# Optimization experiments

Measured on AMD Instinct MI355X. Metric: run time of the kernel, lower is better.

Reference implementation:

```python
import jax, jax.numpy as jnp
import numpy as np

QMAX = 127.0  # int8 symmetric range


def _fake_quant(x, axes):
    """AQT-style int8 symmetric fake-quant over contraction axes.

    Returns quantized integer values (stored as f32) and per-channel scales
    (keepdims over `axes`).
    """
    absmax = jnp.max(jnp.abs(x), axis=axes, keepdims=True)
    scale = jnp.where(absmax > 0, absmax / QMAX, jnp.ones_like(absmax))
    q = jnp.clip(jnp.round(x / scale), -QMAX, QMAX)
    return q, scale


def setup_inputs() -> dict:
    key = jax.random.key(0)
    k1, k2 = jax.random.split(key)
    lhs = jax.random.normal(k1, (4, 16384, 512), dtype=jnp.float32)
    rhs = jax.random.normal(k2, (512, 512), dtype=jnp.float32)
    return {"lhs": lhs, "rhs": rhs}


def reference(lhs, rhs):
    # dimension_numbers = (((2,), (0,)), ((), ())) -- Dense-style contraction.
    # Quantize each operand symmetrically to int8 along its contraction axis.
    lhs_q, lhs_scale = _fake_quant(lhs, axes=(2,))   # lhs_q: [B,S,D], scale: [B,S,1]
    rhs_q, rhs_scale = _fake_quant(rhs, axes=(0,))   # rhs_q: [D,F], scale: [1,F]
    # Integer-valued matmul (accumulation exact in f32 for these magnitudes),
    # then dequantize with the outer product of scales.
    acc = jnp.einsum('bsd,df->bsf', lhs_q, rhs_q)    # [B,S,F]
    return acc * lhs_scale * rhs_scale               # broadcast [B,S,1]*[1,F]
```

## Files before the change

kernel.cpp:

```cpp
#include <hip/hip_runtime.h>
#include <hip/hip_bf16.h>
#include <stdint.h>

#define QMAX 127.0f

typedef __attribute__((ext_vector_type(4))) int i32x4;
typedef __attribute__((ext_vector_type(2))) int i32x2;

typedef __attribute__((address_space(1))) const void GVoid;
typedef __attribute__((address_space(3))) void LVoid;

__device__ inline int quant_i(float x, float inv) {
    float q = rintf(x * inv);
    q = fminf(fmaxf(q, -QMAX), QMAX);
    return (int)q;
}

__device__ inline uint32_t pack4(float4 v, float inv) {
    return (uint32_t)(quant_i(v.x, inv) & 255)
         | ((uint32_t)(quant_i(v.y, inv) & 255) << 8)
         | ((uint32_t)(quant_i(v.z, inv) & 255) << 16)
         | ((uint32_t)(quant_i(v.w, inv) & 255) << 24);
}

__device__ inline float amax8(float4 a, float4 b) {
    return fmaxf(fmaxf(fmaxf(fabsf(a.x), fabsf(a.y)), fmaxf(fabsf(a.z), fabsf(a.w))),
                 fmaxf(fmaxf(fabsf(b.x), fabsf(b.y)), fmaxf(fabsf(b.z), fabsf(b.w))));
}

__global__ void quant_rhs_kernel(const float* __restrict__ rhs,
                                 int8_t* __restrict__ Bt,
                                 float* __restrict__ rscale) {
    const int f = blockIdx.x;
    const int t = threadIdx.x;
    float v[8];
    float amax = 0.f;
#pragma unroll
    for (int i = 0; i < 8; ++i) {
        v[i] = rhs[(size_t)(t + 64 * i) * 512 + f];
        amax = fmaxf(amax, fabsf(v[i]));
    }
#pragma unroll
    for (int m = 1; m <= 32; m <<= 1)
        amax = fmaxf(amax, __shfl_xor(amax, m, 64));
    const float inv = amax > 0.f ? QMAX / amax : 0.f;
    if (t == 0) rscale[f] = amax > 0.f ? amax * (1.0f / QMAX) : 1.0f;
#pragma unroll
    for (int i = 0; i < 8; ++i)
        Bt[(size_t)f * 512 + t + 64 * i] = (int8_t)quant_i(v[i], inv);
}

__global__ __launch_bounds__(256, 8) void quant_lhs_kernel(const float* __restrict__ lhs,
                                                           int8_t* __restrict__ Aq,
                                                           float* __restrict__ lscale) {
    const int lane = threadIdx.x & 63;
    const int wave = threadIdx.x >> 6;
    const int row0 = blockIdx.x * 32 + wave * 8;
    const float* rp = lhs + (size_t)row0 * 512 + lane * 8;
    int8_t* op = Aq + (size_t)row0 * 512 + lane * 8;
#pragma unroll
    for (int r = 0; r < 8; r += 2) {
        const float4 a0 = *(const float4*)(rp + (size_t)r * 512);
        const float4 b0 = *(const float4*)(rp + (size_t)r * 512 + 4);
        const float4 a1 = *(const float4*)(rp + (size_t)(r + 1) * 512);
        const float4 b1 = *(const float4*)(rp + (size_t)(r + 1) * 512 + 4);
        float m0 = amax8(a0, b0);
        float m1 = amax8(a1, b1);
#pragma unroll
        for (int m = 1; m <= 32; m <<= 1) {
            m0 = fmaxf(m0, __shfl_xor(m0, m, 64));
            m1 = fmaxf(m1, __shfl_xor(m1, m, 64));
        }
        const float inv0 = m0 > 0.f ? QMAX / m0 : 0.f;
        const float inv1 = m1 > 0.f ? QMAX / m1 : 0.f;
        if (lane == 0) {
            lscale[row0 + r]     = m0 > 0.f ? m0 * (1.0f / QMAX) : 1.0f;
            lscale[row0 + r + 1] = m1 > 0.f ? m1 * (1.0f / QMAX) : 1.0f;
        }
        i32x2 p0, p1;
        p0.x = (int)pack4(a0, inv0); p0.y = (int)pack4(b0, inv0);
        p1.x = (int)pack4(a1, inv1); p1.y = (int)pack4(b1, inv1);
        *(i32x2*)(op + (size_t)r * 512)       = p0;
        *(i32x2*)(op + (size_t)(r + 1) * 512) = p1;
    }
}

__global__ __launch_bounds__(256, 3) void gemm_kernel(const int8_t* __restrict__ Aq,
                                                      const int8_t* __restrict__ Bt,
                                                      const float* __restrict__ lscale,
                                                      const float* __restrict__ rscale,
                                                      float* __restrict__ out) {
    __shared__ int8_t lds[32768];

    const int tid  = threadIdx.x;
    const int lane = tid & 63;
    const int wave = tid >> 6;
    const int wr   = wave >> 1;
    const int wc   = wave & 1;

    const int g   = blockIdx.x;
    const int xcd = g & 7;
    const int j   = g >> 3;
    const int m0  = (xcd * 64 + (j >> 2)) * 128;
    const int n0  = (j & 3) * 128;

    i32x4 acc[4][4];
#pragma unroll
    for (int i = 0; i < 4; ++i)
#pragma unroll
        for (int jj = 0; jj < 4; ++jj)
            acc[i][jj] = (i32x4){0, 0, 0, 0};

    const int lane15 = lane & 15;
    const int laneHi = lane >> 4;

#pragma unroll
    for (int kt = 0; kt < 512; kt += 128) {
        __syncthreads();
#pragma unroll
        for (int c = 0; c < 4; ++c) {
            const int chunk = (c * 4 + wave) * 1024;
            const int d     = chunk + lane * 16;
            const int row   = d >> 7;
            const int koff  = d & 127;
            const int srck  = koff ^ ((row & 7) << 4);
            const int8_t* srcA = Aq + (size_t)(m0 + row) * 512 + kt + srck;
            __builtin_amdgcn_global_load_lds((GVoid*)srcA, (LVoid*)(lds + chunk), 16, 0, 0);
            const int8_t* srcB = Bt + (size_t)(n0 + row) * 512 + kt + srck;
            __builtin_amdgcn_global_load_lds((GVoid*)srcB, (LVoid*)(lds + 16384 + chunk), 16, 0, 0);
        }
        __syncthreads();

        i32x4 af[4][2], bf[4][2];
#pragma unroll
        for (int mi = 0; mi < 4; ++mi) {
            const int row = wr * 64 + mi * 16 + lane15;
            const int sw  = (row & 7) << 4;
#pragma unroll
            for (int kk = 0; kk < 2; ++kk) {
                const int kb = kk * 64 + laneHi * 16;
                af[mi][kk] = *(const i32x4*)(lds + row * 128 + (kb ^ sw));
            }
        }
#pragma unroll
        for (int ni = 0; ni < 4; ++ni) {
            const int col = wc * 64 + ni * 16 + lane15;
            const int sw  = (col & 7) << 4;
#pragma unroll
            for (int kk = 0; kk < 2; ++kk) {
                const int kb = kk * 64 + laneHi * 16;
                bf[ni][kk] = *(const i32x4*)(lds + 16384 + col * 128 + (kb ^ sw));
            }
        }
#pragma unroll
        for (int kk = 0; kk < 2; ++kk)
#pragma unroll
            for (int mi = 0; mi < 4; ++mi)
#pragma unroll
                for (int ni = 0; ni < 4; ++ni)
                    acc[mi][ni] = __builtin_amdgcn_mfma_i32_16x16x64_i8(
                        af[mi][kk], bf[ni][kk], acc[mi][ni], 0, 0, 0);
    }

    float rs[4];
#pragma unroll
    for (int ni = 0; ni < 4; ++ni)
        rs[ni] = rscale[n0 + wc * 64 + ni * 16 + lane15];
    const int rg = laneHi * 4;
#pragma unroll
    for (int mi = 0; mi < 4; ++mi) {
#pragma unroll
        for (int r = 0; r < 4; ++r) {
            const int grow = m0 + wr * 64 + mi * 16 + rg + r;
            const float ls = lscale[grow];
            float* op = out + (size_t)grow * 512 + n0 + wc * 64;
#pragma unroll
            for (int ni = 0; ni < 4; ++ni)
                op[ni * 16 + lane15] = (float)acc[mi][ni][r] * ls * rs[ni];
        }
    }
}

extern "C" void kernel_launch(void* const* d_in, const int* in_sizes, int n_in,
                              void* d_out, int out_size, void* d_ws, size_t ws_size,
                              hipStream_t stream) {
    const float* lhs = (const float*)d_in[0];
    const float* rhs = (const float*)d_in[1];
    float* out = (float*)d_out;

    char* ws = (char*)d_ws;
    int8_t* Bt    = (int8_t*)ws;
    float* rscale = (float*)(ws + 262144);
    float* lscale = (float*)(ws + 266240);
    int8_t* Aq    = (int8_t*)(ws + 1048576);

    const int rows = in_sizes[0] / 512;

    quant_rhs_kernel<<<512, 64, 0, stream>>>(rhs, Bt, rscale);
    quant_lhs_kernel<<<rows / 32, 256, 0, stream>>>(lhs, Aq, lscale);
    gemm_kernel<<<(rows / 128) * 4, 256, 0, stream>>>(Aq, Bt, lscale, rscale, out);
}
```

Baseline: 73.21 us.

## Fuse quant kernels, double-buffer GEMM LDS, add nontemporal loads/stores

```diff
diff --git a/kernel.cpp b/kernel.cpp
--- a/kernel.cpp
+++ b/kernel.cpp
@@ -4,8 +4,9 @@
 
 #define QMAX 127.0f
 
-typedef __attribute__((ext_vector_type(4))) int i32x4;
-typedef __attribute__((ext_vector_type(2))) int i32x2;
+typedef __attribute__((ext_vector_type(4))) int   i32x4;
+typedef __attribute__((ext_vector_type(2))) int   i32x2;
+typedef __attribute__((ext_vector_type(4))) float f32x4v;
 
 typedef __attribute__((address_space(1))) const void GVoid;
 typedef __attribute__((address_space(3))) void LVoid;
@@ -16,54 +17,58 @@
     return (int)q;
 }
 
-__device__ inline uint32_t pack4(float4 v, float inv) {
+__device__ inline uint32_t pack4(f32x4v v, float inv) {
     return (uint32_t)(quant_i(v.x, inv) & 255)
          | ((uint32_t)(quant_i(v.y, inv) & 255) << 8)
          | ((uint32_t)(quant_i(v.z, inv) & 255) << 16)
          | ((uint32_t)(quant_i(v.w, inv) & 255) << 24);
 }
 
-__device__ inline float amax8(float4 a, float4 b) {
+__device__ inline float amax8(f32x4v a, f32x4v b) {
     return fmaxf(fmaxf(fmaxf(fabsf(a.x), fabsf(a.y)), fmaxf(fabsf(a.z), fabsf(a.w))),
                  fmaxf(fmaxf(fabsf(b.x), fabsf(b.y)), fmaxf(fabsf(b.z), fabsf(b.w))));
 }
 
-__global__ void quant_rhs_kernel(const float* __restrict__ rhs,
-                                 int8_t* __restrict__ Bt,
-                                 float* __restrict__ rscale) {
-    const int f = blockIdx.x;
-    const int t = threadIdx.x;
-    float v[8];
-    float amax = 0.f;
-#pragma unroll
-    for (int i = 0; i < 8; ++i) {
-        v[i] = rhs[(size_t)(t + 64 * i) * 512 + f];
-        amax = fmaxf(amax, fabsf(v[i]));
-    }
-#pragma unroll
-    for (int m = 1; m <= 32; m <<= 1)
-        amax = fmaxf(amax, __shfl_xor(amax, m, 64));
-    const float inv = amax > 0.f ? QMAX / amax : 0.f;
-    if (t == 0) rscale[f] = amax > 0.f ? amax * (1.0f / QMAX) : 1.0f;
-#pragma unroll
-    for (int i = 0; i < 8; ++i)
-        Bt[(size_t)f * 512 + t + 64 * i] = (int8_t)quant_i(v[i], inv);
-}
-
-__global__ __launch_bounds__(256, 8) void quant_lhs_kernel(const float* __restrict__ lhs,
-                                                           int8_t* __restrict__ Aq,
-                                                           float* __restrict__ lscale) {
+__global__ __launch_bounds__(256, 8) void quant_kernel(const float* __restrict__ lhs,
+                                                       const float* __restrict__ rhs,
+                                                       int8_t* __restrict__ Aq,
+                                                       int8_t* __restrict__ Bt,
+                                                       float* __restrict__ lscale,
+                                                       float* __restrict__ rscale,
+                                                       int nLhs) {
     const int lane = threadIdx.x & 63;
     const int wave = threadIdx.x >> 6;
-    const int row0 = blockIdx.x * 32 + wave * 8;
+    const int bid  = blockIdx.x;
+
+    if (bid >= nLhs) {
+        const int f = (bid - nLhs) * 4 + wave;
+        float v[8];
+        float amax = 0.f;
+#pragma unroll
+        for (int i = 0; i < 8; ++i) {
+            v[i] = rhs[(size_t)(lane + 64 * i) * 512 + f];
+            amax = fmaxf(amax, fabsf(v[i]));
+        }
+#pragma unroll
+        for (int m = 1; m <= 32; m <<= 1)
+            amax = fmaxf(amax, __shfl_xor(amax, m, 64));
+        const float inv = amax > 0.f ? QMAX / amax : 0.f;
+        if (lane == 0) rscale[f] = amax > 0.f ? amax * (1.0f / QMAX) : 1.0f;
+#pragma unroll
+        for (int i = 0; i < 8; ++i)
+            Bt[(size_t)f * 512 + lane + 64 * i] = (int8_t)quant_i(v[i], inv);
+        return;
+    }
+
+    const int row0 = bid * 32 + wave * 8;
     const float* rp = lhs + (size_t)row0 * 512 + lane * 8;
     int8_t* op = Aq + (size_t)row0 * 512 + lane * 8;
 #pragma unroll
     for (int r = 0; r < 8; r += 2) {
-        const float4 a0 = *(const float4*)(rp + (size_t)r * 512);
-        const float4 b0 = *(const float4*)(rp + (size_t)r * 512 + 4);
-        const float4 a1 = *(const float4*)(rp + (size_t)(r + 1) * 512);
-        const float4 b1 = *(const float4*)(rp + (size_t)(r + 1) * 512 + 4);
+        const f32x4v a0 = __builtin_nontemporal_load((const f32x4v*)(rp + (size_t)r * 512));
+        const f32x4v b0 = __builtin_nontemporal_load((const f32x4v*)(rp + (size_t)r * 512 + 4));
+        const f32x4v a1 = __builtin_nontemporal_load((const f32x4v*)(rp + (size_t)(r + 1) * 512));
+        const f32x4v b1 = __builtin_nontemporal_load((const f32x4v*)(rp + (size_t)(r + 1) * 512 + 4));
         float m0 = amax8(a0, b0);
         float m1 = amax8(a1, b1);
 #pragma unroll
@@ -85,12 +90,12 @@
     }
 }
 
-__global__ __launch_bounds__(256, 3) void gemm_kernel(const int8_t* __restrict__ Aq,
+__global__ __launch_bounds__(256, 2) void gemm_kernel(const int8_t* __restrict__ Aq,
                                                       const int8_t* __restrict__ Bt,
                                                       const float* __restrict__ lscale,
                                                       const float* __restrict__ rscale,
                                                       float* __restrict__ out) {
-    __shared__ int8_t lds[32768];
+    __shared__ int8_t lds[65536];
 
     const int tid  = threadIdx.x;
     const int lane = tid & 63;
@@ -104,6 +109,10 @@
     const int m0  = (xcd * 64 + (j >> 2)) * 128;
     const int n0  = (j & 3) * 128;
 
+    const int lane15 = lane & 15;
+    const int laneHi = lane >> 4;
+    const int chunkBase = wave * 1024;
+
     i32x4 acc[4][4];
 #pragma unroll
     for (int i = 0; i < 4; ++i)
@@ -111,25 +120,28 @@
         for (int jj = 0; jj < 4; ++jj)
             acc[i][jj] = (i32x4){0, 0, 0, 0};
 
-    const int lane15 = lane & 15;
-    const int laneHi = lane >> 4;
-
-#pragma unroll
-    for (int kt = 0; kt < 512; kt += 128) {
-        __syncthreads();
-#pragma unroll
-        for (int c = 0; c < 4; ++c) {
-            const int chunk = (c * 4 + wave) * 1024;
-            const int d     = chunk + lane * 16;
-            const int row   = d >> 7;
-            const int koff  = d & 127;
-            const int srck  = koff ^ ((row & 7) << 4);
-            const int8_t* srcA = Aq + (size_t)(m0 + row) * 512 + kt + srck;
-            __builtin_amdgcn_global_load_lds((GVoid*)srcA, (LVoid*)(lds + chunk), 16, 0, 0);
-            const int8_t* srcB = Bt + (size_t)(n0 + row) * 512 + kt + srck;
-            __builtin_amdgcn_global_load_lds((GVoid*)srcB, (LVoid*)(lds + 16384 + chunk), 16, 0, 0);
-        }
-        __syncthreads();
+#define STAGE(KT, BUF)                                                              \
+    {                                                                               \
+        _Pragma("unroll")                                                           \
+        for (int c = 0; c < 4; ++c) {                                               \
+            const int chunk = c * 4096 + chunkBase;                                 \
+            const int d     = chunk + lane * 16;                                    \
+            const int row   = d >> 7;                                               \
+            const int srck  = (d & 127) ^ ((row & 7) << 4);                         \
+            const int8_t* sA = Aq + (size_t)(m0 + row) * 512 + (KT) + srck;         \
+            __builtin_amdgcn_global_load_lds((GVoid*)sA, (LVoid*)(lds + (BUF) + chunk), 16, 0, 0); \
+            const int8_t* sB = Bt + (size_t)(n0 + row) * 512 + (KT) + srck;         \
+            __builtin_amdgcn_global_load_lds((GVoid*)sB, (LVoid*)(lds + (BUF) + 16384 + chunk), 16, 0, 0); \
+        }                                                                           \
+    }
+
+    STAGE(0, 0)
+    __syncthreads();
+
+#pragma unroll
+    for (int t = 0; t < 4; ++t) {
+        const int buf = (t & 1) * 32768;
+        if (t < 3) STAGE((t + 1) * 128, (~t & 1) * 32768)
 
         i32x4 af[4][2], bf[4][2];
 #pragma unroll
@@ -139,7 +151,7 @@
 #pragma unroll
             for (int kk = 0; kk < 2; ++kk) {
                 const int kb = kk * 64 + laneHi * 16;
-                af[mi][kk] = *(const i32x4*)(lds + row * 128 + (kb ^ sw));
+                af[mi][kk] = *(const i32x4*)(lds + buf + row * 128 + (kb ^ sw));
             }
         }
 #pragma unroll
@@ -149,7 +161,7 @@
 #pragma unroll
             for (int kk = 0; kk < 2; ++kk) {
                 const int kb = kk * 64 + laneHi * 16;
-                bf[ni][kk] = *(const i32x4*)(lds + 16384 + col * 128 + (kb ^ sw));
+                bf[ni][kk] = *(const i32x4*)(lds + buf + 16384 + col * 128 + (kb ^ sw));
             }
         }
 #pragma unroll
@@ -160,7 +172,10 @@
                 for (int ni = 0; ni < 4; ++ni)
                     acc[mi][ni] = __builtin_amdgcn_mfma_i32_16x16x64_i8(
                         af[mi][kk], bf[ni][kk], acc[mi][ni], 0, 0, 0);
-    }
+
+        if (t < 3) __syncthreads();
+    }
+#undef STAGE
 
     float rs[4];
 #pragma unroll
@@ -176,7 +191,8 @@
             float* op = out + (size_t)grow * 512 + n0 + wc * 64;
 #pragma unroll
             for (int ni = 0; ni < 4; ++ni)
-                op[ni * 16 + lane15] = (float)acc[mi][ni][r] * ls * rs[ni];
+                __builtin_nontemporal_store(acc[mi][ni][r] * ls * rs[ni],
+                                            op + ni * 16 + lane15);
         }
     }
 }
@@ -195,8 +211,8 @@
     int8_t* Aq    = (int8_t*)(ws + 1048576);
 
     const int rows = in_sizes[0] / 512;
-
-    quant_rhs_kernel<<<512, 64, 0, stream>>>(rhs, Bt, rscale);
-    quant_lhs_kernel<<<rows / 32, 256, 0, stream>>>(lhs, Aq, lscale);
+    const int nLhs = rows / 32;
+
+    quant_kernel<<<nLhs + 128, 256, 0, stream>>>(lhs, rhs, Aq, Bt, lscale, rscale, nLhs);
     gemm_kernel<<<(rows / 128) * 4, 256, 0, stream>>>(Aq, Bt, lscale, rscale, out);
 }
```

Result: slower. 77.31 us (+5.6%).
